# Kernel tuning notes

Hardware: AMD Instinct MI355X
Metric: run time of the kernel (lower is better)

The kernel has to match this reference:

```python
import jax, jax.numpy as jnp
import numpy as np

N_HEADS = 16
N_KV_HEADS = 4
HEAD_DIM = 128


def _rope(x, cos, sin):
    # x: [b, s, h, d]; cos/sin: [s, d//2]; interleaved pair rotation
    b, s, h, d = x.shape
    xp = x.reshape(b, s, h, d // 2, 2)
    x_r, x_i = xp[..., 0], xp[..., 1]
    c = cos[None, :, None, :]
    sn = sin[None, :, None, :]
    o_r = x_r * c - x_i * sn
    o_i = x_r * sn + x_i * c
    return jnp.stack([o_r, o_i], axis=-1).reshape(b, s, h, d)


def setup_inputs() -> dict:
    key = jax.random.key(0)
    ks = jax.random.split(key, 7)
    B, S, D = 2, 2048, 2048
    KV = N_KV_HEADS * HEAD_DIM
    x = jax.random.normal(ks[0], (B, S, D), dtype=jnp.float32)
    freqs_cos = jax.random.uniform(ks[1], (S, HEAD_DIM // 2), dtype=jnp.float32)
    freqs_sin = jax.random.uniform(ks[2], (S, HEAD_DIM // 2), dtype=jnp.float32)
    scale = 0.02
    wq = jax.random.normal(ks[3], (D, D), dtype=jnp.float32) * scale
    wk = jax.random.normal(ks[4], (KV, D), dtype=jnp.float32) * scale
    wv = jax.random.normal(ks[5], (KV, D), dtype=jnp.float32) * scale
    wo = jax.random.normal(ks[6], (D, D), dtype=jnp.float32) * scale
    return {"x": x, "freqs_cos": freqs_cos, "freqs_sin": freqs_sin,
            "wq": wq, "wk": wk, "wv": wv, "wo": wo}


def reference(x, freqs_cos, freqs_sin, wq, wk, wv, wo):
    B, S, D = x.shape
    n_rep = N_HEADS // N_KV_HEADS
    q = (x @ wq.T).reshape(B, S, N_HEADS, HEAD_DIM)
    k = (x @ wk.T).reshape(B, S, N_KV_HEADS, HEAD_DIM)
    v = (x @ wv.T).reshape(B, S, N_KV_HEADS, HEAD_DIM)
    q = _rope(q, freqs_cos, freqs_sin)
    k = _rope(k, freqs_cos, freqs_sin)
    # repeat_kv == torch.repeat_interleave along head dim
    k = jnp.repeat(k, n_rep, axis=2)
    v = jnp.repeat(v, n_rep, axis=2)
    q = q.transpose(0, 2, 1, 3)  # [B, H, S, d]
    k = k.transpose(0, 2, 1, 3)
    v = v.transpose(0, 2, 1, 3)
    scale = 1.0 / np.sqrt(HEAD_DIM).astype(np.float32)
    scores = jnp.einsum('bhqd,bhkd->bhqk', q, k) * scale
    causal = jnp.tril(jnp.ones((S, S), dtype=bool))
    scores = jnp.where(causal[None, None], scores, jnp.finfo(jnp.float32).min)
    probs = jax.nn.softmax(scores.astype(jnp.float32), axis=-1).astype(q.dtype)
    out = jnp.einsum('bhqk,bhkd->bhqd', probs, v)
    out = out.transpose(0, 2, 1, 3).reshape(B, S, N_HEADS * HEAD_DIM)
    return out @ wo.T
```

## Files before the change

### kernel.cpp

```cpp
#include <hip/hip_runtime.h>
#include <hip/hip_bf16.h>
#include <type_traits>

using bf16x8 = __attribute__((ext_vector_type(8))) short;
using f32x4  = __attribute__((ext_vector_type(4))) float;
using u16x8  = __attribute__((ext_vector_type(8))) unsigned short;
using u16x4  = __attribute__((ext_vector_type(4))) unsigned short;
using u32x4  = __attribute__((ext_vector_type(4))) unsigned int;

__device__ __forceinline__ float b2f(unsigned short u) {
    unsigned int x = ((unsigned int)u) << 16;
    return __builtin_bit_cast(float, x);
}
__device__ __forceinline__ unsigned short f2b(float f) {
    __hip_bfloat16 h = __float2bfloat16(f);
    return __builtin_bit_cast(unsigned short, h);
}

#if defined(__has_builtin)
#if __has_builtin(__builtin_amdgcn_exp2f)
#define EXP2F(x) __builtin_amdgcn_exp2f(x)
#else
#define EXP2F(x) exp2f(x)
#endif
#else
#define EXP2F(x) exp2f(x)
#endif

__device__ __forceinline__ void async_copy16(const void* g, void* l) {
    __builtin_amdgcn_global_load_lds(
        (const __attribute__((address_space(1))) unsigned int*)g,
        (__attribute__((address_space(3))) unsigned int*)l, 16, 0, 0);
}

#define MFMA16(a, b, c) __builtin_amdgcn_mfma_f32_16x16x32_bf16(a, b, c, 0, 0, 0)

__global__ __launch_bounds__(256) void cvt_f32_to_bf16(
    const float* __restrict__ s, unsigned short* __restrict__ d, int n4)
{
    int i = blockIdx.x * blockDim.x + threadIdx.x;
    if (i >= n4) return;
    float4 v = ((const float4*)s)[i];
    ushort4 o;
    o.x = f2b(v.x); o.y = f2b(v.y); o.z = f2b(v.z); o.w = f2b(v.w);
    ((ushort4*)d)[i] = o;
}

__device__ __forceinline__ void g_stage(
    const unsigned short* __restrict__ A, const unsigned short* __restrict__ Bt,
    unsigned short* As, unsigned short* Bs,
    int k0, int K, int w, int srow, int schunk)
{
    #pragma unroll
    for (int i = 0; i < 4; ++i) {
        int cb = w * 4 + i;
        size_t goff = (size_t)(cb * 8 + srow) * K + k0 + schunk * 8;
        async_copy16(A  + goff, &As[cb * 512]);
        async_copy16(Bt + goff, &Bs[cb * 512]);
    }
}

__device__ __forceinline__ void g_compute(
    const unsigned short* As, const unsigned short* Bs,
    f32x4 (&acc)[4][4], int wm, int wn, int idx, int quad)
{
    #pragma unroll
    for (int ks = 0; ks < 2; ++ks) {
        bf16x8 af[4], bfr[4];
        #pragma unroll
        for (int mi = 0; mi < 4; ++mi) {
            int row = wm + mi * 16 + idx;
            af[mi] = *(const bf16x8*)&As[row * 64 + (((ks * 4 + quad) ^ (row & 7)) * 8)];
        }
        #pragma unroll
        for (int ni = 0; ni < 4; ++ni) {
            int row = wn + ni * 16 + idx;
            bfr[ni] = *(const bf16x8*)&Bs[row * 64 + (((ks * 4 + quad) ^ (row & 7)) * 8)];
        }
        #pragma unroll
        for (int mi = 0; mi < 4; ++mi)
            #pragma unroll
            for (int ni = 0; ni < 4; ++ni)
                acc[mi][ni] = MFMA16(af[mi], bfr[ni], acc[mi][ni]);
    }
}

__global__ __launch_bounds__(256) void qkv_gemm(
    const unsigned short* __restrict__ A,
    const unsigned short* __restrict__ Wq,
    const unsigned short* __restrict__ Wk,
    const unsigned short* __restrict__ Wv,
    unsigned short* __restrict__ Q,
    unsigned short* __restrict__ Kk,
    unsigned short* __restrict__ V)
{
    const int K = 2048;
    constexpr int BK = 64;
    __shared__ unsigned short As0[128 * BK];
    __shared__ unsigned short Bs0[128 * BK];
    __shared__ unsigned short As1[128 * BK];
    __shared__ unsigned short Bs1[128 * BK];

    int tid  = threadIdx.x;
    int w    = tid >> 6;
    int lane = tid & 63;
    int idx  = lane & 15;
    int quad = lane >> 4;
    int wm   = (w >> 1) * 64;
    int wn   = (w & 1) * 64;

    int bm = blockIdx.x / 24;
    int bn = blockIdx.x - bm * 24;
    int m0 = bm * 128;

    const unsigned short* Bt;
    unsigned short* C;
    int Nc, n0;
    if (bn < 16)      { Bt = Wq + (size_t)bn * 128 * K;        C = Q;  Nc = 2048; n0 = bn * 128; }
    else if (bn < 20) { Bt = Wk + (size_t)(bn - 16) * 128 * K; C = Kk; Nc = 512;  n0 = (bn - 16) * 128; }
    else              { Bt = Wv + (size_t)(bn - 20) * 128 * K; C = V;  Nc = 512;  n0 = (bn - 20) * 128; }

    const unsigned short* Ab = A + (size_t)m0 * K;

    int srow   = lane >> 3;
    int schunk = (lane & 7) ^ srow;

    f32x4 acc[4][4];
    #pragma unroll
    for (int mi = 0; mi < 4; ++mi)
        #pragma unroll
        for (int ni = 0; ni < 4; ++ni) acc[mi][ni] = (f32x4){0.f, 0.f, 0.f, 0.f};

    g_stage(Ab, Bt, As0, Bs0, 0, K, w, srow, schunk);
    __syncthreads();

    for (int k0 = 0; k0 < K; k0 += 2 * BK) {
        if (k0 + BK < K)
            g_stage(Ab, Bt, As1, Bs1, k0 + BK, K, w, srow, schunk);
        g_compute(As0, Bs0, acc, wm, wn, idx, quad);
        __syncthreads();
        if (k0 + 2 * BK < K)
            g_stage(Ab, Bt, As0, Bs0, k0 + 2 * BK, K, w, srow, schunk);
        g_compute(As1, Bs1, acc, wm, wn, idx, quad);
        __syncthreads();
    }

    #pragma unroll
    for (int mi = 0; mi < 4; ++mi) {
        #pragma unroll
        for (int r = 0; r < 4; ++r) {
            size_t row = (size_t)(m0 + wm + mi * 16 + quad * 4 + r);
            #pragma unroll
            for (int ni = 0; ni < 4; ++ni) {
                int col = n0 + wn + ni * 16 + idx;
                C[row * Nc + col] = f2b(acc[mi][ni][r]);
            }
        }
    }
}

template <typename OutT>
__global__ __launch_bounds__(256) void gemm_tile(
    const unsigned short* __restrict__ A,
    const unsigned short* __restrict__ Bt,
    OutT* __restrict__ C,
    int M, int N, int K)
{
    constexpr int BK = 64;
    __shared__ unsigned short As0[128 * BK];
    __shared__ unsigned short Bs0[128 * BK];
    __shared__ unsigned short As1[128 * BK];
    __shared__ unsigned short Bs1[128 * BK];

    int tid  = threadIdx.x;
    int w    = tid >> 6;
    int lane = tid & 63;
    int idx  = lane & 15;
    int quad = lane >> 4;
    int wm   = (w >> 1) * 64;
    int wn   = (w & 1) * 64;

    int tilesN = N / 128;
    int bm = blockIdx.x / tilesN;
    int bn = blockIdx.x - bm * tilesN;
    int m0 = bm * 128, n0 = bn * 128;

    const unsigned short* Ab = A  + (size_t)m0 * K;
    const unsigned short* Bb = Bt + (size_t)n0 * K;

    int srow   = lane >> 3;
    int schunk = (lane & 7) ^ srow;

    f32x4 acc[4][4];
    #pragma unroll
    for (int mi = 0; mi < 4; ++mi)
        #pragma unroll
        for (int ni = 0; ni < 4; ++ni) acc[mi][ni] = (f32x4){0.f, 0.f, 0.f, 0.f};

    g_stage(Ab, Bb, As0, Bs0, 0, K, w, srow, schunk);
    __syncthreads();

    for (int k0 = 0; k0 < K; k0 += 2 * BK) {
        if (k0 + BK < K)
            g_stage(Ab, Bb, As1, Bs1, k0 + BK, K, w, srow, schunk);
        g_compute(As0, Bs0, acc, wm, wn, idx, quad);
        __syncthreads();
        if (k0 + 2 * BK < K)
            g_stage(Ab, Bb, As0, Bs0, k0 + 2 * BK, K, w, srow, schunk);
        g_compute(As1, Bs1, acc, wm, wn, idx, quad);
        __syncthreads();
    }

    #pragma unroll
    for (int mi = 0; mi < 4; ++mi) {
        #pragma unroll
        for (int r = 0; r < 4; ++r) {
            size_t row = (size_t)(m0 + wm + mi * 16 + quad * 4 + r);
            #pragma unroll
            for (int ni = 0; ni < 4; ++ni) {
                int col = n0 + wn + ni * 16 + idx;
                if constexpr (std::is_same_v<OutT, float>) {
                    C[row * N + col] = acc[mi][ni][r];
                } else {
                    C[row * N + col] = f2b(acc[mi][ni][r]);
                }
            }
        }
    }
}

__global__ __launch_bounds__(256) void rope_kernel(
    unsigned short* __restrict__ x,
    const float* __restrict__ cs,
    const float* __restrict__ sn,
    int H, int total, float oscale)
{
    int e = blockIdx.x * blockDim.x + threadIdx.x;
    if (e >= total) return;
    int i = e & 63;
    int s = (e / (64 * H)) & 2047;
    float xr = b2f(x[2 * e]);
    float xi = b2f(x[2 * e + 1]);
    float c  = cs[s * 64 + i];
    float sv = sn[s * 64 + i];
    x[2 * e]     = f2b((xr * c - xi * sv) * oscale);
    x[2 * e + 1] = f2b((xr * sv + xi * c) * oscale);
}

__global__ __launch_bounds__(512, 4) void flash_attn(
    const unsigned short* __restrict__ qg,
    const unsigned short* __restrict__ kk,
    const unsigned short* __restrict__ vv,
    unsigned short* __restrict__ out)
{
    const int S = 2048;
    int bid = blockIdx.x;
    int qp  = bid & 15;
    int bh  = bid >> 4;
    int h   = bh & 15;
    int b   = bh >> 4;
    int kvh = h >> 2;

    int p   = b ? (15 - qp) : qp;

    int tid  = threadIdx.x;
    int w    = tid >> 6;
    int lane = tid & 63;
    int idx  = lane & 15;
    int quad = lane >> 4;

    int qt  = 2 * p + (w >> 2);
    int q0  = qt * 64;
    int wq0 = q0 + (w & 3) * 16;
    int qr  = wq0 + idx;

    __shared__ unsigned short Ks[32 * 128];
    __shared__ unsigned short Vt[128 * 40];

    const unsigned short* kbase = kk + ((size_t)b * S * 4 + kvh) * 128;
    const unsigned short* vbase = vv + ((size_t)b * S * 4 + kvh) * 128;

    bf16x8 qf[4];
    {
        const unsigned short* qpp =
            qg + ((size_t)((b * S + wq0 + idx) * 16 + h)) * 128 + quad * 8;
        #pragma unroll
        for (int ko = 0; ko < 4; ++ko)
            qf[ko] = *(const bf16x8*)(qpp + ko * 32);
    }

    f32x4 acc[8];
    #pragma unroll
    for (int n = 0; n < 8; ++n) acc[n] = (f32x4){0.f, 0.f, 0.f, 0.f};
    float lsum = 0.f;

    int dp = (tid & 63) * 2;
    int jb = (tid >> 6) & 3;
    int ih = (tid >> 8) * 4;

    int vcol = (((jb ^ ((dp >> 3) & 3)) << 3) + ih);

    int nt = 4 * p + 4;

    for (int t = 0; t < nt; ++t) {
        {
            int key = w * 4 + (lane >> 4);
            int sc  = (lane & 15) ^ (key & 7);
            async_copy16(kbase + ((size_t)(t * 32 + key)) * 512 + sc * 8,
                         &Ks[w * 512]);
        }
        {
            const unsigned short* vc = vbase + ((size_t)(t * 32 + jb * 4)) * 512 + dp;
            unsigned int ld[4];
            #pragma unroll
            for (int i = 0; i < 4; ++i) {
                int ii  = ih + i;
                int key = (ii >> 1) + 16 * (ii & 1);
                ld[i] = *(const unsigned int*)(vc + key * 512);
            }
            u16x4 lo, hi;
            #pragma unroll
            for (int i = 0; i < 4; ++i) {
                lo[i] = (unsigned short)ld[i];
                hi[i] = (unsigned short)(ld[i] >> 16);
            }
            *(u16x4*)&Vt[dp * 40 + vcol]       = lo;
            *(u16x4*)&Vt[(dp + 1) * 40 + vcol] = hi;
        }
        __syncthreads();

        if (t * 32 <= wq0 + 15) {
            f32x4 s0 = {0.f,0.f,0.f,0.f}, s1 = {0.f,0.f,0.f,0.f};
            #pragma unroll
            for (int ko = 0; ko < 4; ++ko) {
                int kc = ko * 4 + quad;
                bf16x8 kf0 = *(const bf16x8*)&Ks[idx * 128 + ((kc ^ (idx & 7)) * 8)];
                bf16x8 kf1 = *(const bf16x8*)&Ks[(16 + idx) * 128 + ((kc ^ (idx & 7)) * 8)];
                s0 = MFMA16(kf0, qf[ko], s0);
                s1 = MFMA16(kf1, qf[ko], s1);
            }
            unsigned int pk[4];
            if (t * 32 + 31 <= wq0) {
                #pragma unroll
                for (int r = 0; r < 4; ++r) {
                    float p0 = EXP2F(s0[r]);
                    float p1 = EXP2F(s1[r]);
                    lsum += p0 + p1;
                    pk[r] = (unsigned int)f2b(p0) | ((unsigned int)f2b(p1) << 16);
                }
            } else {
                int L = qr - t * 32;
                #pragma unroll
                for (int r = 0; r < 4; ++r) {
                    int kl = quad * 4 + r;
                    float p0 = (kl      <= L) ? EXP2F(s0[r]) : 0.f;
                    float p1 = (kl + 16 <= L) ? EXP2F(s1[r]) : 0.f;
                    lsum += p0 + p1;
                    pk[r] = (unsigned int)f2b(p0) | ((unsigned int)f2b(p1) << 16);
                }
            }
            u32x4 pku = {pk[0], pk[1], pk[2], pk[3]};
            bf16x8 pf = __builtin_bit_cast(bf16x8, pku);
            #pragma unroll
            for (int n = 0; n < 8; ++n) {
                int rr = n * 16 + idx;
                bf16x8 vf = *(const bf16x8*)&Vt[rr * 40 + ((quad ^ ((rr >> 3) & 3)) << 3)];
                acc[n] = MFMA16(vf, pf, acc[n]);
            }
        }
        __syncthreads();
    }

    lsum += __shfl_xor(lsum, 16);
    lsum += __shfl_xor(lsum, 32);
    float inv = 1.f / lsum;
    size_t rowb = (size_t)(b * S + wq0 + idx) * 2048 + h * 128;
    #pragma unroll
    for (int n = 0; n < 8; ++n) {
        ushort4 o;
        o.x = f2b(acc[n][0] * inv);
        o.y = f2b(acc[n][1] * inv);
        o.z = f2b(acc[n][2] * inv);
        o.w = f2b(acc[n][3] * inv);
        *(ushort4*)&out[rowb + n * 16 + quad * 4] = o;
    }
}

extern "C" void kernel_launch(void* const* d_in, const int* in_sizes, int n_in,
                              void* d_out, int out_size, void* d_ws, size_t ws_size,
                              hipStream_t stream)
{
    const float* x  = (const float*)d_in[0];
    const float* fc = (const float*)d_in[1];
    const float* fs = (const float*)d_in[2];
    const float* wq = (const float*)d_in[3];
    const float* wk = (const float*)d_in[4];
    const float* wv = (const float*)d_in[5];
    const float* wo = (const float*)d_in[6];
    float* out = (float*)d_out;

    const int B = 2, S = 2048, D = 2048, KV = 512;
    const int M = B * S;

    unsigned short* ws  = (unsigned short*)d_ws;
    unsigned short* xb  = ws;
    unsigned short* wqb = xb  + (size_t)M * D;
    unsigned short* wkb = wqb + (size_t)D * D;
    unsigned short* wvb = wkb + (size_t)KV * D;
    unsigned short* wob = wvb + (size_t)KV * D;
    unsigned short* qb  = wob + (size_t)D * D;
    unsigned short* kb  = qb  + (size_t)M * D;
    unsigned short* vb  = kb  + (size_t)M * KV;
    unsigned short* ao  = vb  + (size_t)M * KV;

    cvt_f32_to_bf16<<<dim3((M * D / 4) / 256), dim3(256), 0, stream>>>(x,  xb,  M * D / 4);
    cvt_f32_to_bf16<<<dim3((D * D / 4) / 256), dim3(256), 0, stream>>>(wq, wqb, D * D / 4);
    cvt_f32_to_bf16<<<dim3((KV * D / 4) / 256), dim3(256), 0, stream>>>(wk, wkb, KV * D / 4);
    cvt_f32_to_bf16<<<dim3((KV * D / 4) / 256), dim3(256), 0, stream>>>(wv, wvb, KV * D / 4);
    cvt_f32_to_bf16<<<dim3((D * D / 4) / 256), dim3(256), 0, stream>>>(wo, wob, D * D / 4);

    qkv_gemm<<<dim3(768), dim3(256), 0, stream>>>(xb, wqb, wkb, wvb, qb, kb, vb);

    int qpairs = B * S * 16 * 64;
    int kpairs = B * S * 4 * 64;
    const float c2 = 0.12752584f;
    rope_kernel<<<dim3(qpairs / 256), dim3(256), 0, stream>>>(qb, fc, fs, 16, qpairs, c2);
    rope_kernel<<<dim3(kpairs / 256), dim3(256), 0, stream>>>(kb, fc, fs, 4, kpairs, 1.0f);

    flash_attn<<<dim3(512), dim3(512), 0, stream>>>(qb, kb, vb, ao);

    gemm_tile<float><<<dim3((M / 128) * (D / 128)), dim3(256), 0, stream>>>(ao, wob, out, M, D, D);
}
```

Baseline: 322.6 us.

## Rewrite QKV GEMM as 256x256-tile, 8-wave ping-pong pipelined kernel

The QKV projection GEMM moves from 128x128 tiles with 4 waves to 256x256 tiles with 8 waves (512 threads). It uses a hand-scheduled schedule that interleaves async global-to-LDS loads, LDS fragment reads and MFMA bursts, with explicit vmcnt waits, barriers and s_setprio. The block index is also remapped so that neighbouring blocks share operand tiles in cache. The aim is higher arithmetic intensity and better overlap of memory traffic with MFMA work, at the cost of only 192 blocks (less than one wave on a 256-CU part) and heavier register/LDS use.

```diff
diff --git a/kernel.cpp b/kernel.cpp
--- a/kernel.cpp
+++ b/kernel.cpp
@@ -35,6 +35,11 @@
 
 #define MFMA16(a, b, c) __builtin_amdgcn_mfma_f32_16x16x32_bf16(a, b, c, 0, 0, 0)
 
+#define BARRIER() do { asm volatile("" ::: "memory"); \
+    __builtin_amdgcn_s_barrier(); asm volatile("" ::: "memory"); } while (0)
+#define VMCNT6() asm volatile("s_waitcnt vmcnt(6)" ::: "memory")
+#define VMCNT0() asm volatile("s_waitcnt vmcnt(0)" ::: "memory")
+
 __global__ __launch_bounds__(256) void cvt_f32_to_bf16(
     const float* __restrict__ s, unsigned short* __restrict__ d, int n4)
 {
@@ -46,46 +51,7 @@
     ((ushort4*)d)[i] = o;
 }
 
-__device__ __forceinline__ void g_stage(
-    const unsigned short* __restrict__ A, const unsigned short* __restrict__ Bt,
-    unsigned short* As, unsigned short* Bs,
-    int k0, int K, int w, int srow, int schunk)
-{
-    #pragma unroll
-    for (int i = 0; i < 4; ++i) {
-        int cb = w * 4 + i;
-        size_t goff = (size_t)(cb * 8 + srow) * K + k0 + schunk * 8;
-        async_copy16(A  + goff, &As[cb * 512]);
-        async_copy16(Bt + goff, &Bs[cb * 512]);
-    }
-}
-
-__device__ __forceinline__ void g_compute(
-    const unsigned short* As, const unsigned short* Bs,
-    f32x4 (&acc)[4][4], int wm, int wn, int idx, int quad)
-{
-    #pragma unroll
-    for (int ks = 0; ks < 2; ++ks) {
-        bf16x8 af[4], bfr[4];
-        #pragma unroll
-        for (int mi = 0; mi < 4; ++mi) {
-            int row = wm + mi * 16 + idx;
-            af[mi] = *(const bf16x8*)&As[row * 64 + (((ks * 4 + quad) ^ (row & 7)) * 8)];
-        }
-        #pragma unroll
-        for (int ni = 0; ni < 4; ++ni) {
-            int row = wn + ni * 16 + idx;
-            bfr[ni] = *(const bf16x8*)&Bs[row * 64 + (((ks * 4 + quad) ^ (row & 7)) * 8)];
-        }
-        #pragma unroll
-        for (int mi = 0; mi < 4; ++mi)
-            #pragma unroll
-            for (int ni = 0; ni < 4; ++ni)
-                acc[mi][ni] = MFMA16(af[mi], bfr[ni], acc[mi][ni]);
-    }
-}
-
-__global__ __launch_bounds__(256) void qkv_gemm(
+__global__ __launch_bounds__(512, 2) void qkv_gemm(
     const unsigned short* __restrict__ A,
     const unsigned short* __restrict__ Wq,
     const unsigned short* __restrict__ Wk,
@@ -95,67 +61,207 @@
     unsigned short* __restrict__ V)
 {
     const int K = 2048;
-    constexpr int BK = 64;
-    __shared__ unsigned short As0[128 * BK];
-    __shared__ unsigned short Bs0[128 * BK];
-    __shared__ unsigned short As1[128 * BK];
-    __shared__ unsigned short Bs1[128 * BK];
+    __shared__ unsigned short ldsA[2][256 * 64];
+    __shared__ unsigned short ldsB[2][256 * 64];
 
     int tid  = threadIdx.x;
     int w    = tid >> 6;
     int lane = tid & 63;
     int idx  = lane & 15;
     int quad = lane >> 4;
-    int wm   = (w >> 1) * 64;
-    int wn   = (w & 1) * 64;
-
-    int bm = blockIdx.x / 24;
-    int bn = blockIdx.x - bm * 24;
-    int m0 = bm * 128;
+    int srow   = lane >> 3;
+    int schunk = (lane & 7) ^ srow;
+
+    int wfm = (w >> 2) * 64;
+    int wfn = (w & 3) * 64;
+
+    int bid = (blockIdx.x & 7) * 24 + (blockIdx.x >> 3);
+    int bm = bid / 12;
+    int bn = bid - bm * 12;
+    int m0 = bm * 256;
 
     const unsigned short* Bt;
     unsigned short* C;
     int Nc, n0;
-    if (bn < 16)      { Bt = Wq + (size_t)bn * 128 * K;        C = Q;  Nc = 2048; n0 = bn * 128; }
-    else if (bn < 20) { Bt = Wk + (size_t)(bn - 16) * 128 * K; C = Kk; Nc = 512;  n0 = (bn - 16) * 128; }
-    else              { Bt = Wv + (size_t)(bn - 20) * 128 * K; C = V;  Nc = 512;  n0 = (bn - 20) * 128; }
+    if (bn < 8)       { Bt = Wq + (size_t)bn * 256 * K;        C = Q;  Nc = 2048; n0 = bn * 256; }
+    else if (bn < 10) { Bt = Wk + (size_t)(bn - 8) * 256 * K;  C = Kk; Nc = 512;  n0 = (bn - 8) * 256; }
+    else              { Bt = Wv + (size_t)(bn - 10) * 256 * K; C = V;  Nc = 512;  n0 = (bn - 10) * 256; }
 
     const unsigned short* Ab = A + (size_t)m0 * K;
 
-    int srow   = lane >> 3;
-    int schunk = (lane & 7) ^ srow;
-
-    f32x4 acc[4][4];
-    #pragma unroll
-    for (int mi = 0; mi < 4; ++mi)
-        #pragma unroll
-        for (int ni = 0; ni < 4; ++ni) acc[mi][ni] = (f32x4){0.f, 0.f, 0.f, 0.f};
-
-    g_stage(Ab, Bt, As0, Bs0, 0, K, w, srow, schunk);
-    __syncthreads();
-
-    for (int k0 = 0; k0 < K; k0 += 2 * BK) {
-        if (k0 + BK < K)
-            g_stage(Ab, Bt, As1, Bs1, k0 + BK, K, w, srow, schunk);
-        g_compute(As0, Bs0, acc, wm, wn, idx, quad);
-        __syncthreads();
-        if (k0 + 2 * BK < K)
-            g_stage(Ab, Bt, As0, Bs0, k0 + 2 * BK, K, w, srow, schunk);
-        g_compute(As1, Bs1, acc, wm, wn, idx, quad);
-        __syncthreads();
-    }
-
-    #pragma unroll
-    for (int mi = 0; mi < 4; ++mi) {
+    f32x4 acc[8][4];
+    #pragma unroll
+    for (int mf = 0; mf < 8; ++mf)
+        #pragma unroll
+        for (int nf = 0; nf < 4; ++nf) acc[mf][nf] = (f32x4){0.f, 0.f, 0.f, 0.f};
+
+    bf16x8 a[4][2], b0[2][2], b1[2][2];
+
+    auto STAGE = [&](const unsigned short* __restrict__ G, int rb, int kc,
+                     unsigned short* dst) {
+        #pragma unroll
+        for (int i = 0; i < 2; ++i) {
+            int R = (w * 2 + i) * 8;
+            async_copy16(G + (size_t)(rb + R + srow) * K + kc + schunk * 8,
+                         dst + (size_t)R * 64);
+        }
+    };
+    auto LDA = [&](int d, int mh) {
+        #pragma unroll
+        for (int mi = 0; mi < 4; ++mi) {
+            int r = mh * 128 + wfm + mi * 16 + idx;
+            #pragma unroll
+            for (int ks = 0; ks < 2; ++ks)
+                a[mi][ks] = *(const bf16x8*)&ldsA[d][r * 64 + (((ks * 4 + quad) ^ (r & 7)) << 3)];
+        }
+    };
+    auto LDB0 = [&](int d, int nh) {
+        #pragma unroll
+        for (int nj = 0; nj < 2; ++nj) {
+            int r = wfn + nh * 32 + nj * 16 + idx;
+            #pragma unroll
+            for (int ks = 0; ks < 2; ++ks)
+                b0[nj][ks] = *(const bf16x8*)&ldsB[d][r * 64 + (((ks * 4 + quad) ^ (r & 7)) << 3)];
+        }
+    };
+    auto LDB1 = [&](int d, int nh) {
+        #pragma unroll
+        for (int nj = 0; nj < 2; ++nj) {
+            int r = wfn + nh * 32 + nj * 16 + idx;
+            #pragma unroll
+            for (int ks = 0; ks < 2; ++ks)
+                b1[nj][ks] = *(const bf16x8*)&ldsB[d][r * 64 + (((ks * 4 + quad) ^ (r & 7)) << 3)];
+        }
+    };
+    auto MM0 = [&](int mh, int nh) {
+        __builtin_amdgcn_s_setprio(1);
+        #pragma unroll
+        for (int mi = 0; mi < 4; ++mi)
+            #pragma unroll
+            for (int nj = 0; nj < 2; ++nj)
+                #pragma unroll
+                for (int ks = 0; ks < 2; ++ks)
+                    acc[mh * 4 + mi][nh * 2 + nj] =
+                        MFMA16(a[mi][ks], b0[nj][ks], acc[mh * 4 + mi][nh * 2 + nj]);
+        __builtin_amdgcn_s_setprio(0);
+    };
+    auto MM1 = [&](int mh, int nh) {
+        __builtin_amdgcn_s_setprio(1);
+        #pragma unroll
+        for (int mi = 0; mi < 4; ++mi)
+            #pragma unroll
+            for (int nj = 0; nj < 2; ++nj)
+                #pragma unroll
+                for (int ks = 0; ks < 2; ++ks)
+                    acc[mh * 4 + mi][nh * 2 + nj] =
+                        MFMA16(a[mi][ks], b1[nj][ks], acc[mh * 4 + mi][nh * 2 + nj]);
+        __builtin_amdgcn_s_setprio(0);
+    };
+
+    STAGE(Ab, 0,   0,  &ldsA[0][0]);
+    STAGE(Ab, 128, 0,  &ldsA[0][128 * 64]);
+    STAGE(Bt, 0,   0,  &ldsB[0][0]);
+    STAGE(Bt, 128, 0,  &ldsB[0][128 * 64]);
+    STAGE(Ab, 0,   64, &ldsA[1][0]);
+    STAGE(Bt, 0,   64, &ldsB[1][0]);
+    STAGE(Bt, 128, 64, &ldsB[1][128 * 64]);
+    VMCNT6();
+    BARRIER();
+
+    for (int it = 0; it < 15; ++it) {
+        int u = 2 * it;
+        LDA(0, 0); LDB0(0, 0);
+        STAGE(Ab, 128, (u + 1) * 64, &ldsA[1][128 * 64]);
+        BARRIER(); MM0(0, 0); BARRIER();
+        LDB1(0, 1);
+        STAGE(Ab, 0, (u + 2) * 64, &ldsA[0][0]);
+        BARRIER(); MM1(0, 1); BARRIER();
+        LDA(0, 1);
+        STAGE(Bt, 0, (u + 2) * 64, &ldsB[0][0]);
+        BARRIER(); MM1(1, 1); BARRIER();
+        STAGE(Bt, 128, (u + 2) * 64, &ldsB[0][128 * 64]);
+        VMCNT6();
+        BARRIER(); MM0(1, 0); BARRIER();
+        LDA(1, 0); LDB0(1, 0);
+        STAGE(Ab, 128, (u + 2) * 64, &ldsA[0][128 * 64]);
+        BARRIER(); MM0(0, 0); BARRIER();
+        LDB1(1, 1);
+        STAGE(Ab, 0, (u + 3) * 64, &ldsA[1][0]);
+        BARRIER(); MM1(0, 1); BARRIER();
+        LDA(1, 1);
+        STAGE(Bt, 0, (u + 3) * 64, &ldsB[1][0]);
+        BARRIER(); MM1(1, 1); BARRIER();
+        STAGE(Bt, 128, (u + 3) * 64, &ldsB[1][128 * 64]);
+        VMCNT6();
+        BARRIER(); MM0(1, 0); BARRIER();
+    }
+
+    LDA(0, 0); LDB0(0, 0);
+    STAGE(Ab, 128, 31 * 64, &ldsA[1][128 * 64]);
+    BARRIER(); MM0(0, 0); BARRIER();
+    LDB1(0, 1);
+    BARRIER(); MM1(0, 1); BARRIER();
+    LDA(0, 1);
+    BARRIER(); MM1(1, 1); BARRIER();
+    VMCNT0();
+    BARRIER(); MM0(1, 0); BARRIER();
+    LDA(1, 0); LDB0(1, 0);
+    BARRIER(); MM0(0, 0); BARRIER();
+    LDB1(1, 1);
+    BARRIER(); MM1(0, 1); BARRIER();
+    LDA(1, 1);
+    BARRIER(); MM1(1, 1); BARRIER();
+    MM0(1, 0);
+
+    #pragma unroll
+    for (int mf = 0; mf < 8; ++mf) {
         #pragma unroll
         for (int r = 0; r < 4; ++r) {
-            size_t row = (size_t)(m0 + wm + mi * 16 + quad * 4 + r);
-            #pragma unroll
-            for (int ni = 0; ni < 4; ++ni) {
-                int col = n0 + wn + ni * 16 + idx;
-                C[row * Nc + col] = f2b(acc[mi][ni][r]);
-            }
-        }
+            size_t row = (size_t)(m0 + (mf >> 2) * 128 + wfm + (mf & 3) * 16 + quad * 4 + r);
+            #pragma unroll
+            for (int nf = 0; nf < 4; ++nf) {
+                int col = n0 + wfn + nf * 16 + idx;
+                C[row * Nc + col] = f2b(acc[mf][nf][r]);
+            }
+        }
+    }
+}
+
+__device__ __forceinline__ void g_stage(
+    const unsigned short* __restrict__ A, const unsigned short* __restrict__ Bt,
+    unsigned short* As, unsigned short* Bs,
+    int k0, int K, int w, int srow, int schunk)
+{
+    #pragma unroll
+    for (int i = 0; i < 4; ++i) {
+        int cb = w * 4 + i;
+        size_t goff = (size_t)(cb * 8 + srow) * K + k0 + schunk * 8;
+        async_copy16(A  + goff, &As[cb * 512]);
+        async_copy16(Bt + goff, &Bs[cb * 512]);
+    }
+}
+__device__ __forceinline__ void g_compute(
+    const unsigned short* As, const unsigned short* Bs,
+    f32x4 (&acc)[4][4], int wm, int wn, int idx, int quad)
+{
+    #pragma unroll
+    for (int ks = 0; ks < 2; ++ks) {
+        bf16x8 af[4], bfr[4];
+        #pragma unroll
+        for (int mi = 0; mi < 4; ++mi) {
+            int row = wm + mi * 16 + idx;
+            af[mi] = *(const bf16x8*)&As[row * 64 + (((ks * 4 + quad) ^ (row & 7)) * 8)];
+        }
+        #pragma unroll
+        for (int ni = 0; ni < 4; ++ni) {
+            int row = wn + ni * 16 + idx;
+            bfr[ni] = *(const bf16x8*)&Bs[row * 64 + (((ks * 4 + quad) ^ (row & 7)) * 8)];
+        }
+        #pragma unroll
+        for (int mi = 0; mi < 4; ++mi)
+            #pragma unroll
+            for (int ni = 0; ni < 4; ++ni)
+                acc[mi][ni] = MFMA16(af[mi], bfr[ni], acc[mi][ni]);
     }
 }
 
@@ -419,7 +525,7 @@
     cvt_f32_to_bf16<<<dim3((KV * D / 4) / 256), dim3(256), 0, stream>>>(wv, wvb, KV * D / 4);
     cvt_f32_to_bf16<<<dim3((D * D / 4) / 256), dim3(256), 0, stream>>>(wo, wob, D * D / 4);
 
-    qkv_gemm<<<dim3(768), dim3(256), 0, stream>>>(xb, wqb, wkb, wvb, qb, kb, vb);
+    qkv_gemm<<<dim3(192), dim3(512), 0, stream>>>(xb, wqb, wkb, wvb, qb, kb, vb);
 
     int qpairs = B * S * 16 * 64;
     int kpairs = B * S * 4 * 64;
```

After: 326.7 us. About the same (+1.3%).
